# Kernel tuning notes

Measured on AMD Instinct MI355X. Metric: run time of the kernel, lower is better.

Reference implementation:

```python
import jax, jax.numpy as jnp
import numpy as np

VOCAB = 256
D = 512
M = 4            # max_block_size
DS = 2           # downsample_rate
K = 5            # conv kernel size
B = 8
L = 8192


def setup_inputs() -> dict:
    key = jax.random.key(0)
    k1, k2, k3, k4, k5 = jax.random.split(key, 5)
    input_ids = jax.random.randint(k1, (B, L), 0, VOCAB)
    emb = jax.random.normal(k2, (VOCAB, D), dtype=jnp.float32) * 0.02
    emb = emb.at[0].set(0.0)  # padding_idx=0
    conv_w = jax.random.normal(k3, (D, D, K), dtype=jnp.float32) * (1.0 / np.sqrt(D * K))
    conv_b = jax.random.normal(k4, (D,), dtype=jnp.float32) * 0.01
    score_w = jax.random.normal(k5, (D,), dtype=jnp.float32) * (1.0 / np.sqrt(D))
    return {"input_ids": input_ids, "emb": emb, "conv_w": conv_w,
            "conv_b": conv_b, "score_w": score_w}


def _gbst(input_ids, emb, conv_w, conv_b, score_w):
    x = emb[input_ids]                                  # [B, L, D]
    # pre-conv (same padding), NCH layout
    xc = jnp.transpose(x, (0, 2, 1))                    # [B, D, L]
    xc = jax.lax.conv_general_dilated(
        xc, conv_w, window_strides=(1,), padding=[((K - 1) // 2, (K - 1) // 2)],
        dimension_numbers=("NCH", "OIH", "NCH"))
    x = jnp.transpose(xc, (0, 2, 1)) + conv_b           # [B, L, D]

    Lx = x.shape[1]
    cands, scores = [], []
    for b in range(1, M + 1):
        pad = (b - Lx % b) % b
        xp = jnp.pad(x, ((0, 0), (0, pad), (0, 0))) if pad else x
        pooled = xp.reshape(B, -1, b, x.shape[-1]).mean(axis=2)   # [B, Lx/b, D]
        s = pooled @ score_w                                       # [B, Lx/b]
        up = jnp.repeat(pooled, b, axis=1)[:, :Lx]                 # [B, Lx, D]
        us = jnp.repeat(s, b, axis=1)[:, :Lx]                      # [B, Lx]
        cands.append(up)
        scores.append(us)
    candidates = jnp.stack(cands, axis=-1)              # [B, L, D, M]
    block_scores = jax.nn.softmax(jnp.stack(scores, axis=-1), axis=-1)  # [B, L, M]
    latent = jnp.einsum("bldm,blm->bld", candidates, block_scores)      # [B, L, D]

    # final downsample mean-pool
    Ll = latent.shape[1]
    pad = (DS - Ll % DS) % DS
    if pad:
        latent = jnp.pad(latent, ((0, 0), (0, pad), (0, 0)))
    latent = latent.reshape(B, -1, DS, latent.shape[-1]).mean(axis=2)
    return latent                                        # [B, L//DS, D]


def reference(input_ids, emb, conv_w, conv_b, score_w):
    return _gbst(input_ids, emb, conv_w, conv_b, score_w)
```

## Files before the change

### kernel.cpp

```cpp
#include <hip/hip_runtime.h>

#define VOCABN 256
#define DN 512
#define DSN 2
#define KN 5
#define BN 8
#define LN 8192
#define WN 12
#define NW12 ((LN + WN - 1) / WN)
#define NWIN (BN * NW12)
#define LOUTN (LN / DSN)
#define NROWS (KN * VOCABN)
#define ROWB (DN * 2)
#define KPLANE (VOCABN * ROWB)
#define ZOFFB (NROWS * ROWB)
#define SBIAS_IDX (NROWS + 4 * VOCABN + 1)
#define ISP 4

#define GP_BYTES ((size_t)ISP * NROWS * DN * 4)
#define G_OFF GP_BYTES
#define SW_OFF (G_OFF + (size_t)2305 * ROWB)

__device__ inline unsigned short f2bf(float f) {
  unsigned int x = __float_as_uint(f);
  return (unsigned short)((x + 0x7FFFu + ((x >> 16) & 1u)) >> 16);
}

__global__ __launch_bounds__(256) void gbuild_kernel(const float* __restrict__ emb,
                                                     const float* __restrict__ cw,
                                                     float* __restrict__ Gp) {
  const int bx = blockIdx.x;
  const int vt = bx & 3, ot = (bx >> 2) & 7;
  const int kq = bx >> 5;
  const int k = kq % 5, isp = kq / 5;
  const int v0 = vt * 64, o0 = ot * 64;
  const int tid = threadIdx.x;
  const int ox = tid & 15, vx = tid >> 4;
  const int c = tid & 31, rr = tid >> 5;
  __shared__ float se[32][68];
  __shared__ float wt[32][68];
  float acc[4][4] = {};
  for (int ic = 0; ic < 4; ++ic) {
    const int i0 = isp * 128 + ic * 32;
    __syncthreads();
#pragma unroll
    for (int p = 0; p < 8; ++p) {
      const int q = p * 8 + rr;
      se[c][q] = emb[(size_t)(v0 + q) * DN + i0 + c];
      wt[c][q] = cw[((size_t)(o0 + q) * DN + i0 + c) * KN + k];
    }
    __syncthreads();
#pragma unroll
    for (int i = 0; i < 32; ++i) {
      const float4 a = *(const float4*)&se[i][vx * 4];
      const float4 b = *(const float4*)&wt[i][ox * 4];
      acc[0][0] += a.x * b.x; acc[0][1] += a.x * b.y; acc[0][2] += a.x * b.z; acc[0][3] += a.x * b.w;
      acc[1][0] += a.y * b.x; acc[1][1] += a.y * b.y; acc[1][2] += a.y * b.z; acc[1][3] += a.y * b.w;
      acc[2][0] += a.z * b.x; acc[2][1] += a.z * b.y; acc[2][2] += a.z * b.z; acc[2][3] += a.z * b.w;
      acc[3][0] += a.w * b.x; acc[3][1] += a.w * b.y; acc[3][2] += a.w * b.z; acc[3][3] += a.w * b.w;
    }
  }
#pragma unroll
  for (int vi = 0; vi < 4; ++vi) {
    const int row = k * VOCABN + v0 + vx * 4 + vi;
    float4 f;
    f.x = acc[vi][0];
    f.y = acc[vi][1];
    f.z = acc[vi][2];
    f.w = acc[vi][3];
    *(float4*)(Gp + ((size_t)isp * NROWS + row) * DN + o0 + ox * 4) = f;
  }
}

__global__ __launch_bounds__(256) void gswr_kernel(const float* __restrict__ Gp,
                                                   const float* __restrict__ conv_b,
                                                   const float* __restrict__ score_w,
                                                   unsigned int* __restrict__ G32,
                                                   float* __restrict__ SW) {
  const int r = blockIdx.x;
  const int tid = threadIdx.x;
  __shared__ float sred[4];
  if (r >= NROWS && r < NROWS + 5) {
    const int z = NROWS + (r - NROWS) * VOCABN;
    G32[(size_t)z * 256 + tid] = 0u;
    if (tid == 0) SW[z] = 0.f;
    return;
  }
  const float2 sw2 = *(const float2*)(score_w + tid * 2);
  float sdot;
  if (r == NROWS + 5) {
    const float2 cb2 = *(const float2*)(conv_b + tid * 2);
    sdot = cb2.x * sw2.x + cb2.y * sw2.y;
  } else {
    float x = 0.f, y = 0.f;
#pragma unroll
    for (int isp = 0; isp < ISP; ++isp) {
      const float2 p = *(const float2*)(Gp + ((size_t)isp * NROWS + r) * DN + tid * 2);
      x += p.x;
      y += p.y;
    }
    G32[(size_t)r * 256 + tid] = (unsigned)f2bf(x) | ((unsigned)f2bf(y) << 16);
    sdot = x * sw2.x + y * sw2.y;
  }
#pragma unroll
  for (int off = 32; off > 0; off >>= 1) sdot += __shfl_xor(sdot, off, 64);
  if ((tid & 63) == 0) sred[tid >> 6] = sdot;
  __syncthreads();
  if (tid == 0) {
    const float v = sred[0] + sred[1] + sred[2] + sred[3];
    if (r == NROWS + 5) SW[SBIAS_IDX] = v;
    else SW[r] = v;
  }
}

__global__ __launch_bounds__(256, 3) void gbst_main_kernel(const int* __restrict__ ids,
                                                           const unsigned short* __restrict__ G,
                                                           const float* __restrict__ SW,
                                                           const float* __restrict__ conv_b,
                                                           float* __restrict__ out) {
  const int tid = threadIdx.x;
  const int lane = tid & 63;
  const int wave = __builtin_amdgcn_readfirstlane(tid >> 6);
  const int win = blockIdx.x * 4 + wave;
  const int b = win / NW12;
  const int w = win - b * NW12;
  const int l0 = w * WN;

  int joff[WN + 4];
#pragma unroll
  for (int j = 0; j < WN + 4; ++j) {
    const int p = l0 + j - 2;
    const bool v = ((unsigned)p < (unsigned)LN);
    const int a = v ? (b * LN + p) : 0;
    const int id = __builtin_amdgcn_readfirstlane(ids[a]);
    joff[j] = v ? (id * ROWB) : ZOFFB;
  }

  const char* Gc = (const char*)G + lane * 16;
  float y[WN][8];
#pragma unroll
  for (int s = 0; s < WN; ++s) {
#pragma unroll
    for (int c = 0; c < 8; ++c) y[s][c] = 0.f;
#pragma unroll
    for (int kk = 0; kk < KN; ++kk) {
      const uint4 g = *(const uint4*)(Gc + (joff[s + kk] + kk * KPLANE));
      y[s][0] += __uint_as_float(g.x << 16);
      y[s][1] += __uint_as_float(g.x & 0xFFFF0000u);
      y[s][2] += __uint_as_float(g.y << 16);
      y[s][3] += __uint_as_float(g.y & 0xFFFF0000u);
      y[s][4] += __uint_as_float(g.z << 16);
      y[s][5] += __uint_as_float(g.z & 0xFFFF0000u);
      y[s][6] += __uint_as_float(g.w << 16);
      y[s][7] += __uint_as_float(g.w & 0xFFFF0000u);
    }
  }
  float bias[8];
  *(float4*)&bias[0] = *(const float4*)(conv_b + lane * 8);
  *(float4*)&bias[4] = *(const float4*)(conv_b + lane * 8 + 4);
#pragma unroll
  for (int s = 0; s < WN; ++s) {
    const bool valid = (l0 + s) < LN;
#pragma unroll
    for (int c = 0; c < 8; ++c) y[s][c] = valid ? y[s][c] + bias[c] : 0.f;
  }

  const float sbias = SW[SBIAS_IDX];
  float t[WN];
#pragma unroll
  for (int s = 0; s < WN; ++s) {
    float tv = sbias;
#pragma unroll
    for (int kk = 0; kk < KN; ++kk) tv += SW[(joff[s + kk] >> 10) + kk * VOCABN];
    t[s] = (l0 + s < LN) ? tv : 0.f;
  }

#pragma unroll
  for (int jo = 0; jo < WN / 2; ++jo) {
    const int orow = (l0 >> 1) + jo;
    if (orow < LOUTN) {
      float a[8];
#pragma unroll
      for (int c = 0; c < 8; ++c) a[c] = 0.f;
#pragma unroll
      for (int dl = 0; dl < 2; ++dl) {
        const int ll = 2 * jo + dl;
        const float s1 = t[ll];
        const int j2 = ll & ~1;
        const float s2 = 0.5f * (t[j2] + t[j2 + 1]);
        const int j3 = (ll / 3) * 3;
        const float s3 = (1.f / 3.f) * (t[j3] + t[j3 + 1] + t[j3 + 2]);
        const int j4 = ll & ~3;
        const float s4 = 0.25f * (t[j4] + t[j4 + 1] + t[j4 + 2] + t[j4 + 3]);
        const float mx = fmaxf(fmaxf(s1, s2), fmaxf(s3, s4));
        const float e1 = __expf(s1 - mx), e2 = __expf(s2 - mx);
        const float e3 = __expf(s3 - mx), e4 = __expf(s4 - mx);
        const float inv = 1.f / (e1 + e2 + e3 + e4);
        const float c1 = e1 * inv;
        const float c2 = e2 * inv * 0.5f;
        const float c3 = e3 * inv * (1.f / 3.f);
        const float c4 = e4 * inv * 0.25f;
#pragma unroll
        for (int c = 0; c < 8; ++c) {
          a[c] += c1 * y[ll][c] + c2 * (y[j2][c] + y[j2 + 1][c]) +
                  c3 * (y[j3][c] + y[j3 + 1][c] + y[j3 + 2][c]) +
                  c4 * (y[j4][c] + y[j4 + 1][c] + y[j4 + 2][c] + y[j4 + 3][c]);
        }
      }
      float* orow_p = out + ((size_t)b * LOUTN + orow) * DN + lane * 8;
      float4 o0, o1;
      o0.x = 0.5f * a[0]; o0.y = 0.5f * a[1]; o0.z = 0.5f * a[2]; o0.w = 0.5f * a[3];
      o1.x = 0.5f * a[4]; o1.y = 0.5f * a[5]; o1.z = 0.5f * a[6]; o1.w = 0.5f * a[7];
      *(float4*)orow_p = o0;
      *(float4*)(orow_p + 4) = o1;
    }
  }
}

extern "C" void kernel_launch(void* const* d_in, const int* in_sizes, int n_in,
                              void* d_out, int out_size, void* d_ws, size_t ws_size,
                              hipStream_t stream) {
  const int* ids = (const int*)d_in[0];
  const float* emb = (const float*)d_in[1];
  const float* conv_w = (const float*)d_in[2];
  const float* conv_b = (const float*)d_in[3];
  const float* score_w = (const float*)d_in[4];
  float* out = (float*)d_out;

  char* ws = (char*)d_ws;
  float* Gp = (float*)ws;
  unsigned short* G = (unsigned short*)(ws + G_OFF);
  float* SW = (float*)(ws + SW_OFF);

  gbuild_kernel<<<dim3(640), dim3(256), 0, stream>>>(emb, conv_w, Gp);
  gswr_kernel<<<dim3(NROWS + 6), dim3(256), 0, stream>>>(Gp, conv_b, score_w,
                                                         (unsigned int*)G, SW);
  gbst_main_kernel<<<dim3(NWIN / 4), dim3(256), 0, stream>>>(ids, G, SW, conv_b, out);
}
```

Before: 51.71 us.

## Stage bf16 G slices in LDS and precompute softmax coefficients separately

The main kernel now splits D into 8 slices of 64 channels. Each block copies its whole 1280-row bf16 G slice (160KB) into shared memory and then processes a group of windows, gathering from LDS instead of global/L2. Softmax block coefficients are computed once per position by a new coef_kernel and read as float4, and the pooled sums S2/S3/S4 are shared. This adds a kernel launch and a large per-block LDS fill that limits occupancy to one block per CU, and each output element is written as a scalar store.

```diff
diff --git a/kernel.cpp b/kernel.cpp
--- a/kernel.cpp
+++ b/kernel.cpp
@@ -12,14 +12,17 @@
 #define LOUTN (LN / DSN)
 #define NROWS (KN * VOCABN)
 #define ROWB (DN * 2)
-#define KPLANE (VOCABN * ROWB)
-#define ZOFFB (NROWS * ROWB)
 #define SBIAS_IDX (NROWS + 4 * VOCABN + 1)
 #define ISP 4
+#define NSLICE 8
+#define SCH 64
+#define NGRP 32
+#define WPG ((NWIN + NGRP - 1) / NGRP)
 
 #define GP_BYTES ((size_t)ISP * NROWS * DN * 4)
 #define G_OFF GP_BYTES
 #define SW_OFF (G_OFF + (size_t)2305 * ROWB)
+#define COEF_OFF ((size_t)12855552)
 
 __device__ inline unsigned short f2bf(float f) {
   unsigned int x = __float_as_uint(f);
@@ -64,10 +67,7 @@
   for (int vi = 0; vi < 4; ++vi) {
     const int row = k * VOCABN + v0 + vx * 4 + vi;
     float4 f;
-    f.x = acc[vi][0];
-    f.y = acc[vi][1];
-    f.z = acc[vi][2];
-    f.w = acc[vi][3];
+    f.x = acc[vi][0]; f.y = acc[vi][1]; f.z = acc[vi][2]; f.w = acc[vi][3];
     *(float4*)(Gp + ((size_t)isp * NROWS + row) * DN + o0 + ox * 4) = f;
   }
 }
@@ -113,106 +113,131 @@
   }
 }
 
-__global__ __launch_bounds__(256, 3) void gbst_main_kernel(const int* __restrict__ ids,
+__global__ __launch_bounds__(256) void coef_kernel(const int* __restrict__ ids,
+                                                   const float* __restrict__ SW,
+                                                   float4* __restrict__ coefs) {
+  const int bx = blockIdx.x;
+  const int b = bx >> 5;
+  const int p0 = (bx & 31) * 256;
+  const int tid = threadIdx.x;
+  __shared__ float tsh[262];
+  const float sbias = SW[SBIAS_IDX];
+  for (int u = tid; u < 262; u += 256) {
+    const int q = p0 - 3 + u;
+    float tv = 0.f;
+    if ((unsigned)q < (unsigned)LN) {
+      tv = sbias;
+#pragma unroll
+      for (int kk = 0; kk < KN; ++kk) {
+        const int pp = q + kk - 2;
+        const int id = ((unsigned)pp < (unsigned)LN) ? ids[b * LN + pp] : 0;
+        tv += SW[kk * VOCABN + id];
+      }
+    }
+    tsh[u] = tv;
+  }
+  __syncthreads();
+  const int p = p0 + tid;
+  const int base = p0 - 3;
+  const float s1 = tsh[p - base];
+  const int j2 = p & ~1;
+  const float s2 = 0.5f * (tsh[j2 - base] + tsh[j2 + 1 - base]);
+  const int j3 = (p / 3) * 3;
+  const float s3 = (1.f / 3.f) * (tsh[j3 - base] + tsh[j3 + 1 - base] + tsh[j3 + 2 - base]);
+  const int j4 = p & ~3;
+  const float s4 =
+      0.25f * (tsh[j4 - base] + tsh[j4 + 1 - base] + tsh[j4 + 2 - base] + tsh[j4 + 3 - base]);
+  const float mx = fmaxf(fmaxf(s1, s2), fmaxf(s3, s4));
+  const float e1 = __expf(s1 - mx), e2 = __expf(s2 - mx);
+  const float e3 = __expf(s3 - mx), e4 = __expf(s4 - mx);
+  const float inv = 0.5f / (e1 + e2 + e3 + e4);
+  float4 cf;
+  cf.x = e1 * inv;
+  cf.y = e2 * inv * 0.5f;
+  cf.z = e3 * inv * (1.f / 3.f);
+  cf.w = e4 * inv * 0.25f;
+  coefs[(size_t)b * LN + p] = cf;
+}
+
+__global__ __launch_bounds__(512, 1) void gbst_main_kernel(const int* __restrict__ ids,
                                                            const unsigned short* __restrict__ G,
-                                                           const float* __restrict__ SW,
+                                                           const float4* __restrict__ coefs,
                                                            const float* __restrict__ conv_b,
                                                            float* __restrict__ out) {
-  const int tid = threadIdx.x;
-  const int lane = tid & 63;
-  const int wave = __builtin_amdgcn_readfirstlane(tid >> 6);
-  const int win = blockIdx.x * 4 + wave;
-  const int b = win / NW12;
-  const int w = win - b * NW12;
-  const int l0 = w * WN;
-
-  int joff[WN + 4];
-#pragma unroll
-  for (int j = 0; j < WN + 4; ++j) {
-    const int p = l0 + j - 2;
-    const bool v = ((unsigned)p < (unsigned)LN);
-    const int a = v ? (b * LN + p) : 0;
-    const int id = __builtin_amdgcn_readfirstlane(ids[a]);
-    joff[j] = v ? (id * ROWB) : ZOFFB;
-  }
-
-  const char* Gc = (const char*)G + lane * 16;
-  float y[WN][8];
-#pragma unroll
-  for (int s = 0; s < WN; ++s) {
-#pragma unroll
-    for (int c = 0; c < 8; ++c) y[s][c] = 0.f;
-#pragma unroll
-    for (int kk = 0; kk < KN; ++kk) {
-      const uint4 g = *(const uint4*)(Gc + (joff[s + kk] + kk * KPLANE));
-      y[s][0] += __uint_as_float(g.x << 16);
-      y[s][1] += __uint_as_float(g.x & 0xFFFF0000u);
-      y[s][2] += __uint_as_float(g.y << 16);
-      y[s][3] += __uint_as_float(g.y & 0xFFFF0000u);
-      y[s][4] += __uint_as_float(g.z << 16);
-      y[s][5] += __uint_as_float(g.z & 0xFFFF0000u);
-      y[s][6] += __uint_as_float(g.w << 16);
-      y[s][7] += __uint_as_float(g.w & 0xFFFF0000u);
-    }
-  }
-  float bias[8];
-  *(float4*)&bias[0] = *(const float4*)(conv_b + lane * 8);
-  *(float4*)&bias[4] = *(const float4*)(conv_b + lane * 8 + 4);
-#pragma unroll
-  for (int s = 0; s < WN; ++s) {
-    const bool valid = (l0 + s) < LN;
-#pragma unroll
-    for (int c = 0; c < 8; ++c) y[s][c] = valid ? y[s][c] + bias[c] : 0.f;
-  }
-
-  const float sbias = SW[SBIAS_IDX];
-  float t[WN];
-#pragma unroll
-  for (int s = 0; s < WN; ++s) {
-    float tv = sbias;
-#pragma unroll
-    for (int kk = 0; kk < KN; ++kk) tv += SW[(joff[s + kk] >> 10) + kk * VOCABN];
-    t[s] = (l0 + s < LN) ? tv : 0.f;
-  }
-
-#pragma unroll
-  for (int jo = 0; jo < WN / 2; ++jo) {
-    const int orow = (l0 >> 1) + jo;
-    if (orow < LOUTN) {
-      float a[8];
-#pragma unroll
-      for (int c = 0; c < 8; ++c) a[c] = 0.f;
-#pragma unroll
-      for (int dl = 0; dl < 2; ++dl) {
-        const int ll = 2 * jo + dl;
-        const float s1 = t[ll];
-        const int j2 = ll & ~1;
-        const float s2 = 0.5f * (t[j2] + t[j2 + 1]);
-        const int j3 = (ll / 3) * 3;
-        const float s3 = (1.f / 3.f) * (t[j3] + t[j3 + 1] + t[j3 + 2]);
-        const int j4 = ll & ~3;
-        const float s4 = 0.25f * (t[j4] + t[j4 + 1] + t[j4 + 2] + t[j4 + 3]);
-        const float mx = fmaxf(fmaxf(s1, s2), fmaxf(s3, s4));
-        const float e1 = __expf(s1 - mx), e2 = __expf(s2 - mx);
-        const float e3 = __expf(s3 - mx), e4 = __expf(s4 - mx);
-        const float inv = 1.f / (e1 + e2 + e3 + e4);
-        const float c1 = e1 * inv;
-        const float c2 = e2 * inv * 0.5f;
-        const float c3 = e3 * inv * (1.f / 3.f);
-        const float c4 = e4 * inv * 0.25f;
-#pragma unroll
-        for (int c = 0; c < 8; ++c) {
-          a[c] += c1 * y[ll][c] + c2 * (y[j2][c] + y[j2 + 1][c]) +
-                  c3 * (y[j3][c] + y[j3 + 1][c] + y[j3 + 2][c]) +
-                  c4 * (y[j4][c] + y[j4 + 1][c] + y[j4 + 2][c] + y[j4 + 3][c]);
+  __shared__ unsigned short gs[NROWS * SCH];
+  const int bx = blockIdx.x;
+  const int slice = bx & 7;
+  const int grp = bx >> 3;
+  const int tid = threadIdx.x;
+  const int ln = tid & 63;
+  const int wv = tid >> 6;
+
+  const char* Gb = (const char*)G + slice * (SCH * 2);
+#pragma unroll 4
+  for (int pass = 0; pass < 20; ++pass) {
+    const int r = pass * 64 + wv * 8 + (ln >> 3);
+    const uint4 d = *(const uint4*)(Gb + (size_t)r * ROWB + (ln & 7) * 16);
+    *(uint4*)((char*)gs + (size_t)r * (SCH * 2) + (ln & 7) * 16) = d;
+  }
+  __syncthreads();
+
+  const float bias = conv_b[slice * SCH + ln];
+
+  for (int u = wv; u < WPG; u += 8) {
+    const int win0 = grp * WPG + u;
+    if (win0 >= NWIN) break;
+    const int win = __builtin_amdgcn_readfirstlane(win0);
+    const int b = win / NW12;
+    const int ww = win - b * NW12;
+    const int l0 = ww * WN;
+
+    int idv[WN + 4];
+#pragma unroll
+    for (int j = 0; j < WN + 4; ++j) {
+      const int p = l0 + j - 2;
+      const bool tv = ((unsigned)p < (unsigned)LN);
+      idv[j] = tv ? __builtin_amdgcn_readfirstlane(ids[b * LN + (tv ? p : 0)]) : 0;
+    }
+
+    float y[WN];
+#pragma unroll
+    for (int s = 0; s < WN; ++s) {
+      if (l0 + s < LN) {
+        float acc = bias;
+#pragma unroll
+        for (int kk = 0; kk < KN; ++kk) {
+          const unsigned v = gs[(kk * VOCABN + idv[s + kk]) * SCH + ln];
+          acc += __uint_as_float(v << 16);
         }
+        y[s] = acc;
+      } else {
+        y[s] = 0.f;
       }
-      float* orow_p = out + ((size_t)b * LOUTN + orow) * DN + lane * 8;
-      float4 o0, o1;
-      o0.x = 0.5f * a[0]; o0.y = 0.5f * a[1]; o0.z = 0.5f * a[2]; o0.w = 0.5f * a[3];
-      o1.x = 0.5f * a[4]; o1.y = 0.5f * a[5]; o1.z = 0.5f * a[6]; o1.w = 0.5f * a[7];
-      *(float4*)orow_p = o0;
-      *(float4*)(orow_p + 4) = o1;
+    }
+
+    float S2[6], S3[4], S4[3];
+#pragma unroll
+    for (int j = 0; j < 6; ++j) S2[j] = y[2 * j] + y[2 * j + 1];
+#pragma unroll
+    for (int j = 0; j < 4; ++j) S3[j] = y[3 * j] + y[3 * j + 1] + y[3 * j + 2];
+#pragma unroll
+    for (int j = 0; j < 3; ++j) S4[j] = S2[2 * j] + S2[2 * j + 1];
+
+#pragma unroll
+    for (int jo = 0; jo < WN / 2; ++jo) {
+      const int orow = (l0 >> 1) + jo;
+      if (orow < LOUTN) {
+        float a = 0.f;
+#pragma unroll
+        for (int dl = 0; dl < 2; ++dl) {
+          const int ll = 2 * jo + dl;
+          if (l0 + ll < LN) {
+            const float4 cf = coefs[(size_t)b * LN + l0 + ll];
+            a += cf.x * y[ll] + cf.y * S2[jo] + cf.z * S3[ll / 3] + cf.w * S4[jo >> 1];
+          }
+        }
+        out[((size_t)b * LOUTN + orow) * DN + slice * SCH + ln] = a;
+      }
     }
   }
 }
@@ -231,9 +256,11 @@
   float* Gp = (float*)ws;
   unsigned short* G = (unsigned short*)(ws + G_OFF);
   float* SW = (float*)(ws + SW_OFF);
+  float4* coefs = (float4*)(ws + COEF_OFF);
 
   gbuild_kernel<<<dim3(640), dim3(256), 0, stream>>>(emb, conv_w, Gp);
   gswr_kernel<<<dim3(NROWS + 6), dim3(256), 0, stream>>>(Gp, conv_b, score_w,
                                                          (unsigned int*)G, SW);
-  gbst_main_kernel<<<dim3(NWIN / 4), dim3(256), 0, stream>>>(ids, G, SW, conv_b, out);
-}
+  coef_kernel<<<dim3(256), dim3(256), 0, stream>>>(ids, SW, coefs);
+  gbst_main_kernel<<<dim3(256), dim3(512), 0, stream>>>(ids, G, coefs, conv_b, out);
+}
```

Result: slower. 97.81 us (+89.1%).
